# Performance work log

Measured on AMD Instinct MI355X. Metric: run time of the kernel, lower is better.

Reference implementation:

```python
import jax, jax.numpy as jnp
import numpy as np

B, S, D, H, E, O = 8, 2048, 512, 8, 64, 512  # batch, seq, d_in, heads, head_dim, out_dim
NEG_INF = -1e9  # keras Attention adds -1e9 to masked scores


def setup_inputs() -> dict:
    key = jax.random.key(0)
    kq, kk, kv, ko, kx = jax.random.split(key, 5)
    # glorot-uniform-style scale for kernel_size=1 convs (fan_in=D, fan_out=E)
    sqkv = float(np.sqrt(6.0 / (D + E)))
    so = float(np.sqrt(6.0 / (H * E + O)))
    return {
        "query": jax.random.normal(kx, (B, S, D), dtype=jnp.float32),
        "Wq": jax.random.uniform(kq, (H, D, E), jnp.float32, -sqkv, sqkv),
        "Wk": jax.random.uniform(kk, (H, D, E), jnp.float32, -sqkv, sqkv),
        "Wv": jax.random.uniform(kv, (H, D, E), jnp.float32, -sqkv, sqkv),
        "Wo": jax.random.uniform(ko, (H * E, O), jnp.float32, -so, so),
    }


def reference(query, Wq, Wk, Wv, Wo):
    # value defaults to query (self-attention). Conv1D(kernel_size=1, no bias)
    # is a per-timestep linear map; all heads batched into one einsum.
    Q = jnp.einsum('bsd,hde->bhse', query, Wq)
    K = jnp.einsum('bsd,hde->bhse', query, Wk)
    V = jnp.einsum('bsd,hde->bhse', query, Wv)
    # keras Attention(use_scale=False, causal=True): scores = Q K^T (no scale)
    scores = jnp.einsum('bhse,bhte->bhst', Q, K)
    causal = jnp.tril(jnp.ones((S, S), dtype=bool))  # [S, S]
    scores = jnp.where(causal, scores, NEG_INF)
    attn = jax.nn.softmax(scores, axis=-1)
    ctx = jnp.einsum('bhst,bhte->bhse', attn, V)  # [B, H, S, E]
    # concat heads along last axis (head-major), then 1x1 conv projection
    ctx = ctx.transpose(0, 2, 1, 3).reshape(B, S, H * E)
    return jnp.einsum('bsf,fo->bso', ctx, Wo)
```

## Files before the change

kernel.cpp:

```cpp
#include <hip/hip_runtime.h>
#include <stdint.h>

#define Bb 8
#define Ss 2048
#define Dd 512
#define Hh 8
#define Ee 64
#define Oo 512
#define Ff 512
#define Ncat 1536

typedef _Float16 half_t;
typedef __attribute__((ext_vector_type(8))) _Float16 f16x8;
typedef __attribute__((ext_vector_type(4))) float f32x4;
typedef __attribute__((ext_vector_type(16))) float f32x16;
typedef __attribute__((ext_vector_type(4))) float f4;
typedef __attribute__((ext_vector_type(4))) half_t h16x4;
typedef __attribute__((ext_vector_type(4))) unsigned int u32x4;

__device__ __forceinline__ float exp2_fast(float x) {
    float r; asm("v_exp_f32 %0, %1" : "=v"(r) : "v"(x)); return r;
}
__device__ __forceinline__ f32x16 zero16() {
    f32x16 z;
#pragma unroll
    for (int i = 0; i < 16; ++i) z[i] = 0.f;
    return z;
}
__device__ __forceinline__ void gload16(const half_t* g, half_t* l) {
    __builtin_amdgcn_global_load_lds(
        (const __attribute__((address_space(1))) void*)g,
        (__attribute__((address_space(3))) void*)l, 16, 0, 0);
}

__global__ __launch_bounds__(256) void k_cvt_x(const float* __restrict__ x,
                                               half_t* __restrict__ xh) {
    int t = blockIdx.x * 256 + threadIdx.x;
    int s = t >> 6, c = t & 63;
    int cg = c >> 3, cl = c & 7;
    const float* src = x + (size_t)s * Dd + c * 8;
    f4 v0 = *(const f4*)src;
    f4 v1 = *(const f4*)(src + 4);
    union { half_t h[8]; u32x4 u; } o;
#pragma unroll
    for (int j = 0; j < 4; ++j) { o.h[j] = (half_t)v0[j]; o.h[4 + j] = (half_t)v1[j]; }
    int cd = cg * 8 + (cl ^ (s & 7));
    *(u32x4*)(xh + (size_t)s * Dd + cd * 8) = o.u;
}

__global__ __launch_bounds__(256) void k_cvt_w(const float* __restrict__ Wq, const float* __restrict__ Wk,
                                               const float* __restrict__ Wv, const float* __restrict__ Wo,
                                               half_t* __restrict__ Wcat, half_t* __restrict__ WoT) {
    int t = blockIdx.x * 256 + threadIdx.x;
    union { half_t h[8]; u32x4 u; } o;
    if (t < Ncat * 64) {
        int n = t >> 6, dc = t & 63;
        int sel = n >> 9, h = (n >> 6) & 7, e = n & 63;
        const float* W = (sel == 0) ? Wq : (sel == 1) ? Wk : Wv;
        const float* src = W + ((size_t)h * Dd + dc * 8) * Ee + e;
#pragma unroll
        for (int j = 0; j < 8; ++j) o.h[j] = (half_t)src[(size_t)j * Ee];
        int dcs = (dc & ~7) | ((dc & 7) ^ (n & 7));
        *(u32x4*)(Wcat + (size_t)n * Dd + dcs * 8) = o.u;
    } else {
        int u2 = t - Ncat * 64;
        int oo = u2 >> 6, fc = u2 & 63;
        const float* src = Wo + (size_t)(fc * 8) * Oo + oo;
#pragma unroll
        for (int j = 0; j < 8; ++j) o.h[j] = (half_t)src[(size_t)j * Oo];
        int fcs = (fc & ~7) | ((fc & 7) ^ (oo & 7));
        *(u32x4*)(WoT + (size_t)oo * Ff + fcs * 8) = o.u;
    }
}

__global__ __launch_bounds__(256, 2) void k_qkv(const half_t* __restrict__ A,
                                                const half_t* __restrict__ Bw,
                                                half_t* __restrict__ Q,
                                                half_t* __restrict__ K,
                                                half_t* __restrict__ Vt) {
    __shared__ __attribute__((aligned(16))) half_t Ab[2][128 * 64];
    __shared__ __attribute__((aligned(16))) half_t Bbuf[2][128 * 64];

    int bid = blockIdx.x;
    int virt = (bid & 7) * 192 + (bid >> 3);
    int bm = virt / 12, bn = virt % 12;
    int m0 = bm * 128, n0 = bn * 128;

    int wave = threadIdx.x >> 6, lane = threadIdx.x & 63;
    int ar = lane & 15, kg = lane >> 4;
    int wm = wave >> 1, wn = wave & 1;
    int lr = lane >> 3, lc = lane & 7;

    f32x4 acc[4][4];
#pragma unroll
    for (int i = 0; i < 4; ++i)
#pragma unroll
        for (int j = 0; j < 4; ++j) acc[i][j] = (f32x4){0, 0, 0, 0};

#define STAGE_QKV(buf, kt)                                                              \
    {                                                                                   \
        _Pragma("unroll")                                                               \
        for (int i = 0; i < 4; ++i) {                                                   \
            int seg = wave * 4 + i;                                                     \
            int row = seg * 8 + lr;                                                     \
            gload16(A  + (size_t)(m0 + row) * Dd + (kt) * 64 + lc * 8, &Ab[buf][seg * 512]);   \
            gload16(Bw + (size_t)(n0 + row) * Dd + (kt) * 64 + lc * 8, &Bbuf[buf][seg * 512]); \
        }                                                                               \
    }

    STAGE_QKV(0, 0);
    __syncthreads();
    int cur = 0;
    for (int kt = 0; kt < 8; ++kt) {
        if (kt < 7) STAGE_QKV(cur ^ 1, kt + 1);
        f16x8 bf[4][2];
#pragma unroll
        for (int n = 0; n < 4; ++n) {
            int row = wn * 64 + n * 16 + ar;
#pragma unroll
            for (int kh = 0; kh < 2; ++kh)
                bf[n][kh] = *(const f16x8*)&Bbuf[cur][row * 64 + (((kg + kh * 4)) ^ (row & 7)) * 8];
        }
#pragma unroll
        for (int mi = 0; mi < 4; ++mi) {
            int row = wm * 64 + mi * 16 + ar;
            f16x8 a0 = *(const f16x8*)&Ab[cur][row * 64 + ((kg)     ^ (row & 7)) * 8];
            f16x8 a1 = *(const f16x8*)&Ab[cur][row * 64 + ((kg + 4) ^ (row & 7)) * 8];
#pragma unroll
            for (int n = 0; n < 4; ++n) {
                acc[mi][n] = __builtin_amdgcn_mfma_f32_16x16x32_f16(a0, bf[n][0], acc[mi][n], 0, 0, 0);
                acc[mi][n] = __builtin_amdgcn_mfma_f32_16x16x32_f16(a1, bf[n][1], acc[mi][n], 0, 0, 0);
            }
        }
        __syncthreads();
        cur ^= 1;
    }
    int sel = n0 >> 9;
#pragma unroll
    for (int sn = 0; sn < 4; ++sn) {
        int nb = n0 + wn * 64 + sn * 16;
        int h = (nb >> 6) & 7, eb = nb & 63;
#pragma unroll
        for (int mi = 0; mi < 4; ++mi)
#pragma unroll
            for (int r = 0; r < 4; ++r) {
                int sg = m0 + wm * 64 + mi * 16 + kg * 4 + r;
                int bh = (sg >> 11) * 8 + h, sl = sg & 2047;
                half_t val = (half_t)acc[mi][sn][r];
                if (sel == 0)      Q [((size_t)bh * Ss + sl) * Ee + eb + ar] = val;
                else if (sel == 1) K [((size_t)bh * Ss + sl) * Ee + eb + ar] = val;
                else               Vt[((size_t)bh * Ee + eb + ar) * Ss + sl] = val;
            }
    }
#undef STAGE_QKV
}

__global__ __launch_bounds__(256, 4) void k_attn(const half_t* __restrict__ Q,
                                                 const half_t* __restrict__ Kg,
                                                 const half_t* __restrict__ Vtg,
                                                 half_t* __restrict__ ctx) {
    __shared__ __attribute__((aligned(16))) half_t Klds[2][64 * 64];
    __shared__ __attribute__((aligned(16))) half_t Vlds[2][64 * 64];

    int bid = blockIdx.x;
    int xcd = bid & 7;
    int idx = bid >> 3;
    int g   = idx >> 3;
    int g0 = g & 3, j = g >> 2;
    int qb;
    switch (j) {
        case 0:  qb = 15 - g0; break;
        case 1:  qb = 8 + (g0 ^ 2); break;
        case 2:  qb = 4 + g0; break;
        default: qb = g0 ^ 1; break;
    }
    int bh  = xcd * 8 + (idx & 7);

    int wave = threadIdx.x >> 6, lane = threadIdx.x & 63;
    int ql = lane & 31, hi = lane >> 5;
    int qt32 = qb * 4 + wave;
    int qg = qt32 * 32 + ql;

    const half_t* Qb = Q   + (size_t)bh * Ss * Ee;
    const half_t* Kb = Kg  + (size_t)bh * Ss * Ee;
    const half_t* Vb = Vtg + (size_t)bh * Ee * Ss;

    const half_t* qp = Qb + (size_t)qg * Ee + hi * 8;
    f16x8 qf[4];
    const half_t l2e = (half_t)1.44269504f;
#pragma unroll
    for (int d = 0; d < 4; ++d) {
        qf[d] = *(const f16x8*)(qp + d * 16);
#pragma unroll
        for (int jj = 0; jj < 8; ++jj) qf[d][jj] *= l2e;
    }

    f32x16 ot0 = zero16(), ot1 = zero16();
    float m = -1e30f, lp = 0.f;

#define STAGE_KV(buf, kt64)                                                                 \
    {                                                                                       \
        _Pragma("unroll")                                                                   \
        for (int c = 0; c < 2; ++c) {                                                       \
            int seg = 2 * wave + c;                                                         \
            int tK = seg >> 2, dK = seg & 3;                                                \
            gload16(Kb + ((size_t)(kt64) * 64 + tK * 32 + ql) * Ee + dK * 16 + hi * 8,      \
                    &Klds[buf][seg * 512]);                                                 \
            int eh = (seg >> 1) & 1, d2 = seg & 1;                                          \
            gload16(Vb + (size_t)(eh * 32 + ql) * Ss + (kt64) * 64 + tK * 32 + d2 * 16 + hi * 8, \
                    &Vlds[buf][seg * 512]);                                                 \
        }                                                                                   \
    }

    STAGE_KV(0, 0);
    int cur = 0;
    int ktmax64 = qb * 2 + 1;
    for (int kt64 = 0; kt64 <= ktmax64; ++kt64) {
        __syncthreads();
        if (kt64 < ktmax64) STAGE_KV(cur ^ 1, kt64 + 1);
#pragma unroll
        for (int st = 0; st < 2; ++st) {
            int kt32 = kt64 * 2 + st;
            if (kt32 <= qt32) {
                const half_t* Kbase = &Klds[cur][st * 2048];
                const half_t* Vbase = &Vlds[cur][st * 2048];
                f16x8 kf0 = *(const f16x8*)&Kbase[lane * 8];
                f16x8 kf1 = *(const f16x8*)&Kbase[512 + lane * 8];
                f16x8 kf2 = *(const f16x8*)&Kbase[1024 + lane * 8];
                f16x8 kf3 = *(const f16x8*)&Kbase[1536 + lane * 8];

                f32x16 s = zero16();
                __builtin_amdgcn_s_setprio(1);
                s = __builtin_amdgcn_mfma_f32_32x32x16_f16(kf0, qf[0], s, 0, 0, 0);
                s = __builtin_amdgcn_mfma_f32_32x32x16_f16(kf1, qf[1], s, 0, 0, 0);
                s = __builtin_amdgcn_mfma_f32_32x32x16_f16(kf2, qf[2], s, 0, 0, 0);
                s = __builtin_amdgcn_mfma_f32_32x32x16_f16(kf3, qf[3], s, 0, 0, 0);
                __builtin_amdgcn_s_setprio(0);

                if (kt32 == qt32) {
#pragma unroll
                    for (int r = 0; r < 16; ++r) {
                        int kloc = (r & 3) + 8 * (r >> 2) + 4 * hi;
                        if (kloc > ql) s[r] = -1e30f;
                    }
                }

                float m0a = fmaxf(s[0], s[1]),  m1a = fmaxf(s[2], s[3]);
                float m2a = fmaxf(s[4], s[5]),  m3a = fmaxf(s[6], s[7]);
                float m4a = fmaxf(s[8], s[9]),  m5a = fmaxf(s[10], s[11]);
                float m6a = fmaxf(s[12], s[13]), m7a = fmaxf(s[14], s[15]);
                float mb0 = fmaxf(fmaxf(m0a, m1a), fmaxf(m2a, m3a));
                float mb1 = fmaxf(fmaxf(m4a, m5a), fmaxf(m6a, m7a));
                float mt = fmaxf(mb0, mb1);
                mt = fmaxf(mt, __shfl_xor(mt, 32));
                if (!__all(mt <= m + 8.0f)) {
                    float mn = fmaxf(m, mt);
                    float sc = exp2_fast(m - mn);
#pragma unroll
                    for (int r = 0; r < 16; ++r) { ot0[r] *= sc; ot1[r] *= sc; }
                    lp *= sc;
                    m = mn;
                }
                float rs = 0.f;
#pragma unroll
                for (int r = 0; r < 16; ++r) { s[r] = exp2_fast(s[r] - m); rs += s[r]; }
                lp += rs;

                unsigned w[8];
#pragma unroll
                for (int mm = 0; mm < 8; ++mm)
                    asm("v_cvt_pkrtz_f16_f32 %0, %1, %2" : "=v"(w[mm]) : "v"(s[2 * mm]), "v"(s[2 * mm + 1]));
                unsigned t0 = (unsigned)__shfl_xor((int)(hi ? w[0] : w[2]), 32);
                unsigned t1 = (unsigned)__shfl_xor((int)(hi ? w[1] : w[3]), 32);
                unsigned t2 = (unsigned)__shfl_xor((int)(hi ? w[4] : w[6]), 32);
                unsigned t3 = (unsigned)__shfl_xor((int)(hi ? w[5] : w[7]), 32);
                union { unsigned u[4]; f16x8 v; } pb0, pb1;
                pb0.u[0] = hi ? t0 : w[0];  pb0.u[1] = hi ? t1 : w[1];
                pb0.u[2] = hi ? w[2] : t0;  pb0.u[3] = hi ? w[3] : t1;
                pb1.u[0] = hi ? t2 : w[4];  pb1.u[1] = hi ? t3 : w[5];
                pb1.u[2] = hi ? w[6] : t2;  pb1.u[3] = hi ? w[7] : t3;

                f16x8 va00 = *(const f16x8*)&Vbase[lane * 8];
                f16x8 va01 = *(const f16x8*)&Vbase[512 + lane * 8];
                f16x8 va10 = *(const f16x8*)&Vbase[1024 + lane * 8];
                f16x8 va11 = *(const f16x8*)&Vbase[1536 + lane * 8];

                __builtin_amdgcn_s_setprio(1);
                ot0 = __builtin_amdgcn_mfma_f32_32x32x16_f16(va00, pb0.v, ot0, 0, 0, 0);
                ot0 = __builtin_amdgcn_mfma_f32_32x32x16_f16(va01, pb1.v, ot0, 0, 0, 0);
                ot1 = __builtin_amdgcn_mfma_f32_32x32x16_f16(va10, pb0.v, ot1, 0, 0, 0);
                ot1 = __builtin_amdgcn_mfma_f32_32x32x16_f16(va11, pb1.v, ot1, 0, 0, 0);
                __builtin_amdgcn_s_setprio(0);
            }
        }
        cur ^= 1;
    }
#undef STAGE_KV

    float lf = lp + __shfl_xor(lp, 32);
    float inv = 1.0f / lf;
    int b = bh >> 3, h = bh & 7;
    int qs = qg & 7;
    half_t* cb = ctx + ((size_t)b * Ss + qg) * Ff;
#pragma unroll
    for (int gg = 0; gg < 4; ++gg) {
        h16x4 v0, v1;
#pragma unroll
        for (int jj = 0; jj < 4; ++jj) {
            v0[jj] = (half_t)(ot0[gg * 4 + jj] * inv);
            v1[jj] = (half_t)(ot1[gg * 4 + jj] * inv);
        }
        *(h16x4*)(cb + (h * 8 + (gg ^ qs)) * 8 + 4 * hi)       = v0;
        *(h16x4*)(cb + (h * 8 + ((gg + 4) ^ qs)) * 8 + 4 * hi) = v1;
    }
}

__global__ __launch_bounds__(256, 2) void k_proj(const half_t* __restrict__ A,
                                                 const half_t* __restrict__ Bw,
                                                 float* __restrict__ out) {
    __shared__ __attribute__((aligned(16))) half_t Ab[2][128 * 64];
    __shared__ __attribute__((aligned(16))) half_t Bbuf[2][128 * 64];

    int bid = blockIdx.x;
    int virt = (bid & 7) * 64 + (bid >> 3);
    int bm = virt >> 2, bn = virt & 3;
    int m0 = bm * 128, n0 = bn * 128;

    int wave = threadIdx.x >> 6, lane = threadIdx.x & 63;
    int ar = lane & 15, kg = lane >> 4;
    int wm = wave >> 1, wn = wave & 1;
    int lr = lane >> 3, lc = lane & 7;

    f32x4 acc[4][4];
#pragma unroll
    for (int i = 0; i < 4; ++i)
#pragma unroll
        for (int j = 0; j < 4; ++j) acc[i][j] = (f32x4){0, 0, 0, 0};

#define STAGE_PRJ(buf, kt)                                                              \
    {                                                                                   \
        _Pragma("unroll")                                                               \
        for (int i = 0; i < 4; ++i) {                                                   \
            int seg = wave * 4 + i;                                                     \
            int row = seg * 8 + lr;                                                     \
            gload16(A  + (size_t)(m0 + row) * Ff + (kt) * 64 + lc * 8, &Ab[buf][seg * 512]);   \
            gload16(Bw + (size_t)(n0 + row) * Ff + (kt) * 64 + lc * 8, &Bbuf[buf][seg * 512]); \
        }                                                                               \
    }

    STAGE_PRJ(0, 0);
    __syncthreads();
    int cur = 0;
    for (int kt = 0; kt < 8; ++kt) {
        if (kt < 7) STAGE_PRJ(cur ^ 1, kt + 1);
        f16x8 bf[4][2];
#pragma unroll
        for (int n = 0; n < 4; ++n) {
            int row = wn * 64 + n * 16 + ar;
#pragma unroll
            for (int kh = 0; kh < 2; ++kh)
                bf[n][kh] = *(const f16x8*)&Bbuf[cur][row * 64 + (((kg + kh * 4)) ^ (row & 7)) * 8];
        }
#pragma unroll
        for (int mi = 0; mi < 4; ++mi) {
            int row = wm * 64 + mi * 16 + ar;
            f16x8 a0 = *(const f16x8*)&Ab[cur][row * 64 + ((kg)     ^ (row & 7)) * 8];
            f16x8 a1 = *(const f16x8*)&Ab[cur][row * 64 + ((kg + 4) ^ (row & 7)) * 8];
#pragma unroll
            for (int n = 0; n < 4; ++n) {
                acc[mi][n] = __builtin_amdgcn_mfma_f32_16x16x32_f16(a0, bf[n][0], acc[mi][n], 0, 0, 0);
                acc[mi][n] = __builtin_amdgcn_mfma_f32_16x16x32_f16(a1, bf[n][1], acc[mi][n], 0, 0, 0);
            }
        }
        __syncthreads();
        cur ^= 1;
    }
#pragma unroll
    for (int sn = 0; sn < 4; ++sn)
#pragma unroll
        for (int mi = 0; mi < 4; ++mi)
#pragma unroll
            for (int r = 0; r < 4; ++r) {
                int sg = m0 + wm * 64 + mi * 16 + kg * 4 + r;
                out[(size_t)sg * Oo + n0 + wn * 64 + sn * 16 + ar] = acc[mi][sn][r];
            }
#undef STAGE_PRJ
}

extern "C" void kernel_launch(void* const* d_in, const int* in_sizes, int n_in,
                              void* d_out, int out_size, void* d_ws, size_t ws_size,
                              hipStream_t stream) {
    const float* x  = (const float*)d_in[0];
    const float* Wq = (const float*)d_in[1];
    const float* Wk = (const float*)d_in[2];
    const float* Wv = (const float*)d_in[3];
    const float* Wo = (const float*)d_in[4];
    float* out = (float*)d_out;

    char* ws = (char*)d_ws;
    size_t off = 0;
    half_t* xh   = (half_t*)(ws + off); off += (size_t)Bb * Ss * Dd * 2;
    half_t* Wcat = (half_t*)(ws + off); off += (size_t)Ncat * Dd * 2;
    half_t* WoT  = (half_t*)(ws + off); off += (size_t)Oo * Ff * 2;
    half_t* Qd   = (half_t*)(ws + off); off += (size_t)Bb * Hh * Ss * Ee * 2;
    half_t* Kd   = (half_t*)(ws + off); off += (size_t)Bb * Hh * Ss * Ee * 2;
    half_t* Vtd  = (half_t*)(ws + off); off += (size_t)Bb * Hh * Ss * Ee * 2;
    half_t* ctx  = (half_t*)(ws + off); off += (size_t)Bb * Ss * Ff * 2;

    k_cvt_x<<<4096, 256, 0, stream>>>(x, xh);
    k_cvt_w<<<512, 256, 0, stream>>>(Wq, Wk, Wv, Wo, Wcat, WoT);
    k_qkv<<<1536, 256, 0, stream>>>(xh, Wcat, Qd, Kd, Vtd);
    k_attn<<<1024, 256, 0, stream>>>(Qd, Kd, Vtd, ctx);
    k_proj<<<512, 256, 0, stream>>>(ctx, WoT, out);
}
```

Before: 152.6 us.

## Split attention KV range across two wave groups with LDS merge

Each attention block doubles to 512 threads. Two groups of four waves each process half of the key/value tiles for the same query rows, in 32-key tiles with per-group double-buffered LDS. The partial softmax states (output accumulators, max, and sum) are then merged through shared memory before the normalized context is written. This targets the serial length of the causal KV loop by splitting each query block's work across more waves. The cost is an extra LDS merge, more shared memory per block, more barriers, and uneven split work, since the second group's tiles are partly masked.

```diff
diff --git a/kernel.cpp b/kernel.cpp
--- a/kernel.cpp
+++ b/kernel.cpp
@@ -155,12 +155,13 @@
 #undef STAGE_QKV
 }
 
-__global__ __launch_bounds__(256, 4) void k_attn(const half_t* __restrict__ Q,
+__global__ __launch_bounds__(512, 8) void k_attn(const half_t* __restrict__ Q,
                                                  const half_t* __restrict__ Kg,
                                                  const half_t* __restrict__ Vtg,
                                                  half_t* __restrict__ ctx) {
-    __shared__ __attribute__((aligned(16))) half_t Klds[2][64 * 64];
-    __shared__ __attribute__((aligned(16))) half_t Vlds[2][64 * 64];
+    __shared__ __attribute__((aligned(16))) char smem[35072];
+    half_t* stg = (half_t*)smem;
+    float*  mrg = (float*)smem;
 
     int bid = blockIdx.x;
     int xcd = bid & 7;
@@ -174,11 +175,12 @@
         case 2:  qb = 4 + g0; break;
         default: qb = g0 ^ 1; break;
     }
-    int bh  = xcd * 8 + (idx & 7);
+    int bh = xcd * 8 + (idx & 7);
 
     int wave = threadIdx.x >> 6, lane = threadIdx.x & 63;
+    int grp = wave >> 2, w4 = wave & 3;
     int ql = lane & 31, hi = lane >> 5;
-    int qt32 = qb * 4 + wave;
+    int qt32 = qb * 4 + w4;
     int qg = qt32 * 32 + ql;
 
     const half_t* Qb = Q   + (size_t)bh * Ss * Ee;
@@ -198,120 +200,141 @@
     f32x16 ot0 = zero16(), ot1 = zero16();
     float m = -1e30f, lp = 0.f;
 
-#define STAGE_KV(buf, kt64)                                                                 \
-    {                                                                                       \
-        _Pragma("unroll")                                                                   \
-        for (int c = 0; c < 2; ++c) {                                                       \
-            int seg = 2 * wave + c;                                                         \
-            int tK = seg >> 2, dK = seg & 3;                                                \
-            gload16(Kb + ((size_t)(kt64) * 64 + tK * 32 + ql) * Ee + dK * 16 + hi * 8,      \
-                    &Klds[buf][seg * 512]);                                                 \
-            int eh = (seg >> 1) & 1, d2 = seg & 1;                                          \
-            gload16(Vb + (size_t)(eh * 32 + ql) * Ss + (kt64) * 64 + tK * 32 + d2 * 16 + hi * 8, \
-                    &Vlds[buf][seg * 512]);                                                 \
-        }                                                                                   \
-    }
-
-    STAGE_KV(0, 0);
+    int SL = qb * 2 + 2;
+    int tbase = grp * SL;
+    half_t* reg0 = stg + (grp * 2 + 0) * 4096;
+    half_t* reg1 = stg + (grp * 2 + 1) * 4096;
+    int sgb = w4 * 2;
+
+#define STAGE_KV(buf, tile)                                                               \
+    {                                                                                     \
+        half_t* rg = (buf) ? reg1 : reg0;                                                 \
+        _Pragma("unroll")                                                                 \
+        for (int c = 0; c < 2; ++c) {                                                     \
+            int s = sgb + c;                                                              \
+            if (s < 4) {                                                                  \
+                gload16(Kb + ((size_t)(tile) * 32 + ql) * Ee + s * 16 + hi * 8,           \
+                        rg + s * 512);                                                    \
+            } else {                                                                      \
+                int s2 = s - 4, eh = s2 >> 1, d2 = s2 & 1;                                \
+                gload16(Vb + (size_t)(eh * 32 + ql) * Ss + (tile) * 32 + d2 * 16 + hi * 8,\
+                        rg + 2048 + s2 * 512);                                            \
+            }                                                                             \
+        }                                                                                 \
+    }
+
+    STAGE_KV(0, tbase);
     int cur = 0;
-    int ktmax64 = qb * 2 + 1;
-    for (int kt64 = 0; kt64 <= ktmax64; ++kt64) {
+    for (int t = 0; t < SL; ++t) {
         __syncthreads();
-        if (kt64 < ktmax64) STAGE_KV(cur ^ 1, kt64 + 1);
-#pragma unroll
-        for (int st = 0; st < 2; ++st) {
-            int kt32 = kt64 * 2 + st;
-            if (kt32 <= qt32) {
-                const half_t* Kbase = &Klds[cur][st * 2048];
-                const half_t* Vbase = &Vlds[cur][st * 2048];
-                f16x8 kf0 = *(const f16x8*)&Kbase[lane * 8];
-                f16x8 kf1 = *(const f16x8*)&Kbase[512 + lane * 8];
-                f16x8 kf2 = *(const f16x8*)&Kbase[1024 + lane * 8];
-                f16x8 kf3 = *(const f16x8*)&Kbase[1536 + lane * 8];
-
-                f32x16 s = zero16();
-                __builtin_amdgcn_s_setprio(1);
-                s = __builtin_amdgcn_mfma_f32_32x32x16_f16(kf0, qf[0], s, 0, 0, 0);
-                s = __builtin_amdgcn_mfma_f32_32x32x16_f16(kf1, qf[1], s, 0, 0, 0);
-                s = __builtin_amdgcn_mfma_f32_32x32x16_f16(kf2, qf[2], s, 0, 0, 0);
-                s = __builtin_amdgcn_mfma_f32_32x32x16_f16(kf3, qf[3], s, 0, 0, 0);
-                __builtin_amdgcn_s_setprio(0);
-
-                if (kt32 == qt32) {
-#pragma unroll
-                    for (int r = 0; r < 16; ++r) {
-                        int kloc = (r & 3) + 8 * (r >> 2) + 4 * hi;
-                        if (kloc > ql) s[r] = -1e30f;
-                    }
+        if (t + 1 < SL) STAGE_KV(cur ^ 1, tbase + t + 1);
+        int kt32 = tbase + t;
+        if (kt32 <= qt32) {
+            half_t* rg = cur ? reg1 : reg0;
+            f16x8 kf0 = *(const f16x8*)(rg + lane * 8);
+            f16x8 kf1 = *(const f16x8*)(rg + 512 + lane * 8);
+            f16x8 kf2 = *(const f16x8*)(rg + 1024 + lane * 8);
+            f16x8 kf3 = *(const f16x8*)(rg + 1536 + lane * 8);
+
+            f32x16 s = zero16();
+            __builtin_amdgcn_s_setprio(1);
+            s = __builtin_amdgcn_mfma_f32_32x32x16_f16(kf0, qf[0], s, 0, 0, 0);
+            s = __builtin_amdgcn_mfma_f32_32x32x16_f16(kf1, qf[1], s, 0, 0, 0);
+            s = __builtin_amdgcn_mfma_f32_32x32x16_f16(kf2, qf[2], s, 0, 0, 0);
+            s = __builtin_amdgcn_mfma_f32_32x32x16_f16(kf3, qf[3], s, 0, 0, 0);
+            __builtin_amdgcn_s_setprio(0);
+
+            if (kt32 == qt32) {
+#pragma unroll
+                for (int r = 0; r < 16; ++r) {
+                    int kloc = (r & 3) + 8 * (r >> 2) + 4 * hi;
+                    if (kloc > ql) s[r] = -1e30f;
                 }
-
-                float m0a = fmaxf(s[0], s[1]),  m1a = fmaxf(s[2], s[3]);
-                float m2a = fmaxf(s[4], s[5]),  m3a = fmaxf(s[6], s[7]);
-                float m4a = fmaxf(s[8], s[9]),  m5a = fmaxf(s[10], s[11]);
-                float m6a = fmaxf(s[12], s[13]), m7a = fmaxf(s[14], s[15]);
-                float mb0 = fmaxf(fmaxf(m0a, m1a), fmaxf(m2a, m3a));
-                float mb1 = fmaxf(fmaxf(m4a, m5a), fmaxf(m6a, m7a));
-                float mt = fmaxf(mb0, mb1);
-                mt = fmaxf(mt, __shfl_xor(mt, 32));
-                if (!__all(mt <= m + 8.0f)) {
-                    float mn = fmaxf(m, mt);
-                    float sc = exp2_fast(m - mn);
-#pragma unroll
-                    for (int r = 0; r < 16; ++r) { ot0[r] *= sc; ot1[r] *= sc; }
-                    lp *= sc;
-                    m = mn;
-                }
-                float rs = 0.f;
-#pragma unroll
-                for (int r = 0; r < 16; ++r) { s[r] = exp2_fast(s[r] - m); rs += s[r]; }
-                lp += rs;
-
-                unsigned w[8];
-#pragma unroll
-                for (int mm = 0; mm < 8; ++mm)
-                    asm("v_cvt_pkrtz_f16_f32 %0, %1, %2" : "=v"(w[mm]) : "v"(s[2 * mm]), "v"(s[2 * mm + 1]));
-                unsigned t0 = (unsigned)__shfl_xor((int)(hi ? w[0] : w[2]), 32);
-                unsigned t1 = (unsigned)__shfl_xor((int)(hi ? w[1] : w[3]), 32);
-                unsigned t2 = (unsigned)__shfl_xor((int)(hi ? w[4] : w[6]), 32);
-                unsigned t3 = (unsigned)__shfl_xor((int)(hi ? w[5] : w[7]), 32);
-                union { unsigned u[4]; f16x8 v; } pb0, pb1;
-                pb0.u[0] = hi ? t0 : w[0];  pb0.u[1] = hi ? t1 : w[1];
-                pb0.u[2] = hi ? w[2] : t0;  pb0.u[3] = hi ? w[3] : t1;
-                pb1.u[0] = hi ? t2 : w[4];  pb1.u[1] = hi ? t3 : w[5];
-                pb1.u[2] = hi ? w[6] : t2;  pb1.u[3] = hi ? w[7] : t3;
-
-                f16x8 va00 = *(const f16x8*)&Vbase[lane * 8];
-                f16x8 va01 = *(const f16x8*)&Vbase[512 + lane * 8];
-                f16x8 va10 = *(const f16x8*)&Vbase[1024 + lane * 8];
-                f16x8 va11 = *(const f16x8*)&Vbase[1536 + lane * 8];
-
-                __builtin_amdgcn_s_setprio(1);
-                ot0 = __builtin_amdgcn_mfma_f32_32x32x16_f16(va00, pb0.v, ot0, 0, 0, 0);
-                ot0 = __builtin_amdgcn_mfma_f32_32x32x16_f16(va01, pb1.v, ot0, 0, 0, 0);
-                ot1 = __builtin_amdgcn_mfma_f32_32x32x16_f16(va10, pb0.v, ot1, 0, 0, 0);
-                ot1 = __builtin_amdgcn_mfma_f32_32x32x16_f16(va11, pb1.v, ot1, 0, 0, 0);
-                __builtin_amdgcn_s_setprio(0);
-            }
+            }
+
+            float m0a = fmaxf(s[0], s[1]),  m1a = fmaxf(s[2], s[3]);
+            float m2a = fmaxf(s[4], s[5]),  m3a = fmaxf(s[6], s[7]);
+            float m4a = fmaxf(s[8], s[9]),  m5a = fmaxf(s[10], s[11]);
+            float m6a = fmaxf(s[12], s[13]), m7a = fmaxf(s[14], s[15]);
+            float mt = fmaxf(fmaxf(fmaxf(m0a, m1a), fmaxf(m2a, m3a)),
+                             fmaxf(fmaxf(m4a, m5a), fmaxf(m6a, m7a)));
+            mt = fmaxf(mt, __shfl_xor(mt, 32));
+            if (!__all(mt <= m + 8.0f)) {
+                float mn = fmaxf(m, mt);
+                float sc = exp2_fast(m - mn);
+#pragma unroll
+                for (int r = 0; r < 16; ++r) { ot0[r] *= sc; ot1[r] *= sc; }
+                lp *= sc;
+                m = mn;
+            }
+            float rs = 0.f;
+#pragma unroll
+            for (int r = 0; r < 16; ++r) { s[r] = exp2_fast(s[r] - m); rs += s[r]; }
+            lp += rs;
+
+            unsigned w[8];
+#pragma unroll
+            for (int mm = 0; mm < 8; ++mm)
+                asm("v_cvt_pkrtz_f16_f32 %0, %1, %2" : "=v"(w[mm]) : "v"(s[2 * mm]), "v"(s[2 * mm + 1]));
+            unsigned t0 = (unsigned)__shfl_xor((int)(hi ? w[0] : w[2]), 32);
+            unsigned t1 = (unsigned)__shfl_xor((int)(hi ? w[1] : w[3]), 32);
+            unsigned t2 = (unsigned)__shfl_xor((int)(hi ? w[4] : w[6]), 32);
+            unsigned t3 = (unsigned)__shfl_xor((int)(hi ? w[5] : w[7]), 32);
+            union { unsigned u[4]; f16x8 v; } pb0, pb1;
+            pb0.u[0] = hi ? t0 : w[0];  pb0.u[1] = hi ? t1 : w[1];
+            pb0.u[2] = hi ? w[2] : t0;  pb0.u[3] = hi ? w[3] : t1;
+            pb1.u[0] = hi ? t2 : w[4];  pb1.u[1] = hi ? t3 : w[5];
+            pb1.u[2] = hi ? w[6] : t2;  pb1.u[3] = hi ? w[7] : t3;
+
+            f16x8 va0 = *(const f16x8*)(rg + 2048 + lane * 8);
+            f16x8 va1 = *(const f16x8*)(rg + 2560 + lane * 8);
+            f16x8 va2 = *(const f16x8*)(rg + 3072 + lane * 8);
+            f16x8 va3 = *(const f16x8*)(rg + 3584 + lane * 8);
+
+            __builtin_amdgcn_s_setprio(1);
+            ot0 = __builtin_amdgcn_mfma_f32_32x32x16_f16(va0, pb0.v, ot0, 0, 0, 0);
+            ot0 = __builtin_amdgcn_mfma_f32_32x32x16_f16(va1, pb1.v, ot0, 0, 0, 0);
+            ot1 = __builtin_amdgcn_mfma_f32_32x32x16_f16(va2, pb0.v, ot1, 0, 0, 0);
+            ot1 = __builtin_amdgcn_mfma_f32_32x32x16_f16(va3, pb1.v, ot1, 0, 0, 0);
+            __builtin_amdgcn_s_setprio(0);
         }
         cur ^= 1;
     }
 #undef STAGE_KV
 
-    float lf = lp + __shfl_xor(lp, 32);
-    float inv = 1.0f / lf;
-    int b = bh >> 3, h = bh & 7;
-    int qs = qg & 7;
-    half_t* cb = ctx + ((size_t)b * Ss + qg) * Ff;
-#pragma unroll
-    for (int gg = 0; gg < 4; ++gg) {
-        h16x4 v0, v1;
-#pragma unroll
-        for (int jj = 0; jj < 4; ++jj) {
-            v0[jj] = (half_t)(ot0[gg * 4 + jj] * inv);
-            v1[jj] = (half_t)(ot1[gg * 4 + jj] * inv);
-        }
-        *(h16x4*)(cb + (h * 8 + (gg ^ qs)) * 8 + 4 * hi)       = v0;
-        *(h16x4*)(cb + (h * 8 + ((gg + 4) ^ qs)) * 8 + 4 * hi) = v1;
+    __syncthreads();
+    if (grp) {
+        float* p = mrg + ((size_t)(w4 * 64 + lane)) * 34;
+#pragma unroll
+        for (int r = 0; r < 16; ++r) { p[r] = ot0[r]; p[16 + r] = ot1[r]; }
+        p[32] = m; p[33] = lp;
+    }
+    __syncthreads();
+    if (!grp) {
+        float* p = mrg + ((size_t)(w4 * 64 + lane)) * 34;
+        float m2 = p[32], lp2 = p[33];
+        float mn = fmaxf(m, m2);
+        float sA = exp2_fast(m - mn);
+        float sB = exp2_fast(m2 - mn);
+        float lpm = lp * sA + lp2 * sB;
+        float lf = lpm + __shfl_xor(lpm, 32);
+        float inv = 1.0f / lf;
+        int b = bh >> 3, h = bh & 7;
+        int qs = qg & 7;
+        half_t* cb = ctx + ((size_t)b * Ss + qg) * Ff;
+#pragma unroll
+        for (int gg = 0; gg < 4; ++gg) {
+            h16x4 v0, v1;
+#pragma unroll
+            for (int jj = 0; jj < 4; ++jj) {
+                float o0 = ot0[gg * 4 + jj] * sA + p[gg * 4 + jj] * sB;
+                float o1 = ot1[gg * 4 + jj] * sA + p[16 + gg * 4 + jj] * sB;
+                v0[jj] = (half_t)(o0 * inv);
+                v1[jj] = (half_t)(o1 * inv);
+            }
+            *(h16x4*)(cb + (h * 8 + (gg ^ qs)) * 8 + 4 * hi)       = v0;
+            *(h16x4*)(cb + (h * 8 + ((gg + 4) ^ qs)) * 8 + 4 * hi) = v1;
+        }
     }
 }
 
@@ -410,6 +433,6 @@
     k_cvt_x<<<4096, 256, 0, stream>>>(x, xh);
     k_cvt_w<<<512, 256, 0, stream>>>(Wq, Wk, Wv, Wo, Wcat, WoT);
     k_qkv<<<1536, 256, 0, stream>>>(xh, Wcat, Qd, Kd, Vtd);
-    k_attn<<<1024, 256, 0, stream>>>(Qd, Kd, Vtd, ctx);
+    k_attn<<<1024, 512, 0, stream>>>(Qd, Kd, Vtd, ctx);
     k_proj<<<512, 256, 0, stream>>>(ctx, WoT, out);
 }
```

Result: slower. 594.9 us (+289.7%).
